# Kernel tuning notes

Measured on AMD Instinct MI355X. Metric: run time of the kernel, lower is better.

Reference implementation:

```python
import jax, jax.numpy as jnp
import numpy as np

N_HEAD, D_K, D_V = 8, 64, 64
TOPK = 16
B, N_R, N_W = 256, 64, 64
D_READ = D_WRITE = D_OUT = 512
TEMP = float(np.power(D_K, 0.5))
EPS = 1e-7  # 10e-8 in original Sparse_attention


def sparse_attention(a, top_k):
    # a: (rows, n); RIMs Sparse_attention: threshold at k-th largest, clamp, renormalize
    if a.shape[-1] <= top_k:
        return a
    delta = jax.lax.top_k(a, top_k)[0][..., -1:] + EPS
    w = jnp.clip(a - delta, 0.0, None)
    return w / (jnp.sum(w, axis=-1, keepdims=True) + EPS)


def setup_inputs() -> dict:
    key = jax.random.key(0)
    ks = jax.random.split(key, 8)
    q = jax.random.normal(ks[0], (B, N_R, D_READ), dtype=jnp.float32)
    k = jax.random.normal(ks[1], (B, N_W, D_WRITE), dtype=jnp.float32)
    v = jax.random.normal(ks[2], (B, N_W, D_WRITE), dtype=jnp.float32)
    # GroupLinearLayer weights: (num_blocks, d_in, n_head*d)
    Wq = 0.02 * jax.random.normal(ks[3], (N_R, D_READ, N_HEAD * D_K), dtype=jnp.float32)
    Wk = 0.02 * jax.random.normal(ks[4], (N_W, D_WRITE, N_HEAD * D_K), dtype=jnp.float32)
    Wv = 0.02 * jax.random.normal(ks[5], (N_W, D_WRITE, N_HEAD * D_V), dtype=jnp.float32)
    fc_w = 0.02 * jax.random.normal(ks[6], (D_OUT, N_HEAD * D_V), dtype=jnp.float32)
    fc_b = jnp.zeros((D_OUT,), dtype=jnp.float32)
    gate_w = 0.02 * jax.random.normal(ks[7], (D_OUT, N_HEAD * D_V), dtype=jnp.float32)
    gate_b = jnp.zeros((D_OUT,), dtype=jnp.float32)
    return {"q": q, "k": k, "v": v, "Wq": Wq, "Wk": Wk, "Wv": Wv,
            "fc_w": fc_w, "fc_b": fc_b, "gate_w": gate_w, "gate_b": gate_b}


def reference(q, k, v, Wq, Wk, Wv, fc_w, fc_b, gate_w, gate_b):
    # grouped per-block projections: out[b,n] = x[b,n] @ W[n]
    qp = jnp.einsum('bnd,nde->bne', q, Wq).reshape(B, N_R, N_HEAD, D_K)
    kp = jnp.einsum('bnd,nde->bne', k, Wk).reshape(B, N_W, N_HEAD, D_K)
    vp = jnp.einsum('bnd,nde->bne', v, Wv).reshape(B, N_W, N_HEAD, D_V)
    # (H*B, len, d) with head-major leading dim, matching permute(2,0,1,3).view(-1,...)
    qh = qp.transpose(2, 0, 1, 3).reshape(N_HEAD * B, N_R, D_K)
    kh = kp.transpose(2, 0, 1, 3).reshape(N_HEAD * B, N_W, D_K)
    vh = vp.transpose(2, 0, 1, 3).reshape(N_HEAD * B, N_W, D_V)
    scores = jnp.einsum('ijk,ilk->ijl', qh, kh) / TEMP          # (HB, Nr, Nw)
    a = jnp.exp(jnp.max(scores, axis=-1, keepdims=True))        # (HB, Nr, 1)
    # flag=True: softmax over the query-block dim (permute/softmax/reshape)
    a = jax.nn.softmax(a[..., 0], axis=-1)                      # (HB, Nr)
    a = sparse_attention(a, TOPK)                               # (HB, Nr)
    attn = a[..., None]                                         # (HB, Nr, 1)
    # einsum 'ijk,ikl->ijl' with attn's k-dim == 1 broadcasts: attn * sum_k v
    out = attn * jnp.sum(vh, axis=1, keepdims=True)             # (HB, Nr, Dv)
    out = out.reshape(N_HEAD, B, N_R, D_V).transpose(1, 2, 0, 3).reshape(B, N_R, N_HEAD * D_V)
    fc_out = out @ fc_w.T + fc_b
    gate = jax.nn.sigmoid(out @ gate_w.T + gate_b)
    output = gate * jnp.tanh(fc_out)                            # residual=True gating
    return output
```

## Files before the change

kernel.cpp:

```cpp
#include <hip/hip_runtime.h>
#include <stdint.h>

#define B_    256
#define NR    64
#define NW    64
#define DIN   512
#define NH    8
#define DK    64
#define E_    512
#define TEMP_INV 0.125f
#define EPSV  1e-7f

typedef unsigned short u16;
typedef unsigned int   u32;
typedef _Float16 f16;
typedef __attribute__((ext_vector_type(2))) float    floatx2;
typedef __attribute__((ext_vector_type(4))) float    floatx4;
typedef __attribute__((ext_vector_type(4))) u32      uintx4;
typedef __attribute__((ext_vector_type(2))) _Float16 halfx2;
typedef __attribute__((ext_vector_type(8))) _Float16 halfx8;

__device__ __forceinline__ halfx2 h2(u32 u) { union { u32 u; halfx2 h; } c; c.u = u; return c.h; }
__device__ __forceinline__ u32 pkh(float a, float b) {
    union { halfx2 h; u32 u; } c; c.h = (halfx2){(f16)a, (f16)b}; return c.u;
}


#define STORE_A(sbuf, pa) do {                                                \
        u32 hh_[8];                                                           \
        _Pragma("unroll")                                                     \
        for (int c = 0; c < 4; c++) {                                         \
            hh_[2*c]   = pkh(pa[c].x, pa[c].y);                               \
            hh_[2*c+1] = pkh(pa[c].z, pa[c].w);                               \
        }                                                                     \
        *(uintx4*)&As[sbuf][(2*ahalf+0)*1024 + arow*8] =                      \
            (uintx4){hh_[0],hh_[1],hh_[2],hh_[3]};                            \
        *(uintx4*)&As[sbuf][(2*ahalf+1)*1024 + arow*8] =                      \
            (uintx4){hh_[4],hh_[5],hh_[6],hh_[7]};                            \
    } while (0)

#define STORE_B(sbuf, pb) do {                                                \
        _Pragma("unroll")                                                     \
        for (int eo = 0; eo < 2; eo++) {                                      \
            uintx4 hv_ = (uintx4){pkh(pb[0][eo], pb[1][eo]),                  \
                                  pkh(pb[2][eo], pb[3][eo]),                  \
                                  pkh(pb[4][eo], pb[5][eo]),                  \
                                  pkh(pb[6][eo], pb[7][eo])};                 \
            *(uintx4*)&Bs[sbuf][kq * 1024 + eo * 512 + p * 8] = hv_;          \
        }                                                                     \
    } while (0)

#define LOAD_A(pa, kn) do {                                                   \
        _Pragma("unroll")                                                     \
        for (int c = 0; c < 4; c++)                                           \
            pa[c] = *(const floatx4*)(aptr + (kn) + c * 4);                   \
    } while (0)

#define LOAD_B(pb, kn) do {                                                   \
        _Pragma("unroll")                                                     \
        for (int j = 0; j < 8; j++)                                           \
            pb[j] = *(const floatx2*)(wptr + (size_t)((kn) + kq*8 + j) * E_); \
    } while (0)

#define COMPUTE(sbuf) do {                                                    \
        halfx8 af_[4], bf_[4];                                                \
        _Pragma("unroll")                                                     \
        for (int mi = 0; mi < 4; mi++)                                        \
            af_[mi] = *(const halfx8*)&As[sbuf][quad*1024 + (wm + mi*16 + l15)*8]; \
        _Pragma("unroll")                                                     \
        for (int ni = 0; ni < 4; ni++) {                                      \
            int e_ = wn + ni*16 + l15;                                        \
            bf_[ni] = *(const halfx8*)&Bs[sbuf][quad*1024 + (e_&1)*512 + (e_>>1)*8]; \
        }                                                                     \
        _Pragma("unroll")                                                     \
        for (int mi = 0; mi < 4; mi++)                                        \
            _Pragma("unroll")                                                 \
            for (int ni = 0; ni < 4; ni++)                                    \
                acc[mi][ni] = __builtin_amdgcn_mfma_f32_16x16x32_f16(         \
                    af_[mi], bf_[ni], acc[mi][ni], 0, 0, 0);                  \
    } while (0)

#define PHASE_BARRIER() do {                                                  \
        asm volatile("s_waitcnt lgkmcnt(0)" ::: "memory");                    \
        __builtin_amdgcn_s_barrier();                                         \
        __builtin_amdgcn_sched_barrier(0);                                    \
    } while (0)

__global__ __launch_bounds__(256, 2)
void proj_kernel(const float* __restrict__ q, const float* __restrict__ kk_,
                 const float* __restrict__ v,
                 const float* __restrict__ Wq, const float* __restrict__ Wk,
                 const float* __restrict__ Wv,
                 f16* __restrict__ qp, f16* __restrict__ kp,
                 f16* __restrict__ vp, float* __restrict__ vsum)
{
    const float* X; const float* W; f16* dst;
    if (blockIdx.z == 0)      { X = q;   W = Wq; dst = qp; }
    else if (blockIdx.z == 1) { X = kk_; W = Wk; dst = kp; }
    else                      { X = v;   W = Wv; dst = vp; }

    const int n  = blockIdx.x * 8 + (blockIdx.y & 7);
    const int t_ = blockIdx.y >> 3;
    const int m0 = (t_ >> 2) * 128;
    const int n0 = (t_ & 3) * 128;

    __shared__ u16 As[2][4096];
    __shared__ u16 Bs[2][4096];

    const int tid  = threadIdx.x;
    const int lane = tid & 63;
    const int wave = tid >> 6;
    const int wm   = (wave >> 1) * 64;
    const int wn   = (wave & 1) * 64;
    const int l15  = lane & 15;
    const int quad = lane >> 4;

    floatx4 acc[4][4];
#pragma unroll
    for (int i = 0; i < 4; i++)
#pragma unroll
        for (int j = 0; j < 4; j++) acc[i][j] = (floatx4){0.f, 0.f, 0.f, 0.f};

    const int arow  = tid >> 1;
    const int ahalf = tid & 1;
    const float* aptr = X + ((size_t)(m0 + arow) * NW + n) * DIN + ahalf * 16;
    const int kq = tid >> 6;
    const int p  = tid & 63;
    const float* wptr = W + (size_t)n * (DIN * E_) + n0 + 2 * p;

    floatx4 pa0[4], pa1[4];
    floatx2 pb0[8], pb1[8];

    LOAD_A(pa0, 0);
    LOAD_A(pa1, 32);
    LOAD_B(pb0, 0);
    LOAD_B(pb1, 32);

#pragma unroll 1
    for (int it2 = 0; it2 < 8; it2++) {
        const int k0 = it2 * 64;
        STORE_A(0, pa0);
        STORE_B(0, pb0);
        if (it2 < 7) { LOAD_A(pa0, k0 + 64); LOAD_B(pb0, k0 + 64); }
        PHASE_BARRIER();
        COMPUTE(0);
        STORE_A(1, pa1);
        STORE_B(1, pb1);
        if (it2 < 7) { LOAD_A(pa1, k0 + 96); LOAD_B(pb1, k0 + 96); }
        PHASE_BARRIER();
        COMPUTE(1);
    }

    if (dst) {
#pragma unroll
        for (int mi = 0; mi < 4; mi++) {
            int rowb = m0 + wm + mi * 16 + quad * 4;
#pragma unroll
            for (int ni = 0; ni < 4; ni++) {
                int col = n0 + wn + ni * 16 + l15;
#pragma unroll
                for (int r = 0; r < 4; r++)
                    dst[((size_t)(rowb + r) * NW + n) * E_ + col] = (f16)acc[mi][ni][r];
            }
        }
    } else {
#pragma unroll
        for (int mi = 0; mi < 4; mi++) {
            int rowb = m0 + wm + mi * 16 + quad * 4;
#pragma unroll
            for (int ni = 0; ni < 4; ni++) {
                int col = n0 + wn + ni * 16 + l15;
#pragma unroll
                for (int r = 0; r < 4; r++)
                    atomicAdd(&vsum[(size_t)(rowb + r) * E_ + col], acc[mi][ni][r]);
            }
        }
    }
}

__global__ __launch_bounds__(256)
void vsum_kernel(const f16* __restrict__ vp, float* __restrict__ vsum)
{
    const int b = blockIdx.x;
    const int t = threadIdx.x;
    const u32* src = (const u32*)vp + (size_t)b * NW * (E_ / 2) + t;
    float s0 = 0.f, s1 = 0.f;
#pragma unroll 4
    for (int nn = 0; nn < NW; nn++) {
        halfx2 hv = h2(src[(size_t)nn * (E_ / 2)]);
        s0 += (float)hv.x;
        s1 += (float)hv.y;
    }
    *(floatx2*)&vsum[(size_t)b * E_ + 2 * t] = (floatx2){s0, s1};
}

__global__ __launch_bounds__(256)
void attn_kernel(const f16* __restrict__ qp, const f16* __restrict__ kp,
                 float* __restrict__ attnT)
{
    const int h = blockIdx.x >> 8;
    const int b = blockIdx.x & 255;
    __shared__ u16 qs[64 * 72];
    __shared__ u16 ks[64 * 72];
    __shared__ float ms[64];

    const int t    = threadIdx.x;
    const int w    = t >> 6;
    const int lane = t & 63;
    const int l15  = lane & 15;
    const int quad = lane >> 4;

    {
        const int r = t >> 2, c = t & 3;
        const f16* qsrc = qp + ((size_t)(b * NR + r)) * E_ + h * DK + c * 16;
        const f16* ksrc = kp + ((size_t)(b * NW + r)) * E_ + h * DK + c * 16;
        *(uintx4*)&qs[r * 72 + c * 16]     = *(const uintx4*)(qsrc);
        *(uintx4*)&qs[r * 72 + c * 16 + 8] = *(const uintx4*)(qsrc + 8);
        *(uintx4*)&ks[r * 72 + c * 16]     = *(const uintx4*)(ksrc);
        *(uintx4*)&ks[r * 72 + c * 16 + 8] = *(const uintx4*)(ksrc + 8);
    }
    __syncthreads();

    floatx4 sc[4];
#pragma unroll
    for (int ni = 0; ni < 4; ni++) sc[ni] = (floatx4){0.f, 0.f, 0.f, 0.f};

    halfx8 af[2];
#pragma unroll
    for (int kk = 0; kk < 2; kk++)
        af[kk] = *(const halfx8*)&qs[(w * 16 + l15) * 72 + kk * 32 + quad * 8];
#pragma unroll
    for (int ni = 0; ni < 4; ni++)
#pragma unroll
        for (int kk = 0; kk < 2; kk++) {
            halfx8 bf = *(const halfx8*)&ks[(ni * 16 + l15) * 72 + kk * 32 + quad * 8];
            sc[ni] = __builtin_amdgcn_mfma_f32_16x16x32_f16(af[kk], bf, sc[ni], 0, 0, 0);
        }

#pragma unroll
    for (int r = 0; r < 4; r++) {
        float rm = fmaxf(fmaxf(sc[0][r], sc[1][r]), fmaxf(sc[2][r], sc[3][r]));
#pragma unroll
        for (int d = 1; d < 16; d <<= 1) rm = fmaxf(rm, __shfl_xor(rm, d));
        if (l15 == 0) ms[w * 16 + quad * 4 + r] = rm;
    }
    __syncthreads();

    if (t < 64) {
        float mm = ms[lane] * TEMP_INV;
        float e = expf(mm);
        float mx = e;
#pragma unroll
        for (int d = 1; d < 64; d <<= 1) mx = fmaxf(mx, __shfl_xor(mx, d));
        float tt = expf(e - mx);
        float S = tt;
#pragma unroll
        for (int d = 1; d < 64; d <<= 1) S += __shfl_xor(S, d);
        float s = tt / S;

        float cur = s, v16 = 0.f;
        for (int itk = 0; itk < 16; itk++) {
            float mv = cur;
#pragma unroll
            for (int d = 1; d < 64; d <<= 1) mv = fmaxf(mv, __shfl_xor(mv, d));
            unsigned long long bal = __ballot(cur == mv);
            int first = __ffsll(bal) - 1;
            if (lane == first) cur = -1e30f;
            v16 = mv;
        }
        float delta = v16 + EPSV;
        float ww = fmaxf(s - delta, 0.f);
        float sw = ww;
#pragma unroll
        for (int d = 1; d < 64; d <<= 1) sw += __shfl_xor(sw, d);
        attnT[((size_t)b * NR + lane) * NH + h] = ww / (sw + EPSV);
    }
}

__global__ __launch_bounds__(256)
void fcv_kernel(const float* __restrict__ vsum, const float* __restrict__ fc_w,
                const float* __restrict__ gate_w, float* __restrict__ fcv,
                float* __restrict__ gatev)
{
    const int ohalf = blockIdx.x >> 3;
    const int bq    = blockIdx.x & 7;
    const int h     = blockIdx.y;
    const float* W  = blockIdx.z ? gate_w : fc_w;
    float* out      = blockIdx.z ? gatev : fcv;
    const int o     = ohalf * 256 + threadIdx.x;

    __shared__ float vs[32 * 64];
#pragma unroll
    for (int i = 0; i < 8; i++) {
        int idx = i * 256 + threadIdx.x;
        int bb = idx >> 6, d = idx & 63;
        vs[idx] = vsum[(size_t)(bq * 32 + bb) * E_ + h * DK + d];
    }
    floatx4 wr[16];
#pragma unroll
    for (int c = 0; c < 16; c++)
        wr[c] = *(const floatx4*)(W + (size_t)o * E_ + h * DK + c * 4);
    __syncthreads();

    for (int bb = 0; bb < 32; bb++) {
        const floatx4* vr = (const floatx4*)&vs[bb * 64];
        float a = 0.f;
#pragma unroll
        for (int c = 0; c < 16; c++) {
            floatx4 vv = vr[c];
            a += vv.x * wr[c].x + vv.y * wr[c].y + vv.z * wr[c].z + vv.w * wr[c].w;
        }
        out[((size_t)(bq * 32 + bb) * NH + h) * E_ + o] = a;
    }
}

__global__ __launch_bounds__(256)
void final_kernel(const float* __restrict__ fcv, const float* __restrict__ gatev,
                  const float* __restrict__ attnT, const float* __restrict__ fc_b,
                  const float* __restrict__ gate_b, float* __restrict__ out)
{
    const int b   = blockIdx.x;
    const int r0  = blockIdx.y * 16;
    const int tid = threadIdx.x;
    __shared__ float ats[16 * NH];

    if (tid < 16 * NH) ats[tid] = attnT[(size_t)b * NR * NH + r0 * NH + tid];

    float fr[2][8], gr[2][8];
#pragma unroll
    for (int half = 0; half < 2; half++) {
        int o = half * 256 + tid;
#pragma unroll
        for (int hh = 0; hh < 8; hh++) {
            fr[half][hh] = fcv[((size_t)b * NH + hh) * E_ + o];
            gr[half][hh] = gatev[((size_t)b * NH + hh) * E_ + o];
        }
    }
    float bfc0 = fc_b[tid],   bfc1 = fc_b[256 + tid];
    float bgt0 = gate_b[tid], bgt1 = gate_b[256 + tid];
    __syncthreads();

    for (int r = 0; r < 16; r++) {
        float a[8];
#pragma unroll
        for (int hh = 0; hh < 8; hh++) a[hh] = ats[r * NH + hh];
#pragma unroll
        for (int half = 0; half < 2; half++) {
            int o = half * 256 + tid;
            float fc = half ? bfc1 : bfc0;
            float gt = half ? bgt1 : bgt0;
#pragma unroll
            for (int hh = 0; hh < 8; hh++) {
                fc = fmaf(a[hh], fr[half][hh], fc);
                gt = fmaf(a[hh], gr[half][hh], gt);
            }
            float g  = 1.f / (1.f + __expf(-gt));
            float e2 = __expf(2.f * fc);
            float th = 1.f - 2.f / (e2 + 1.f);
            out[((size_t)(b * NR + r0 + r)) * E_ + o] = g * th;
        }
    }
}

extern "C" void kernel_launch(void* const* d_in, const int* in_sizes, int n_in,
                              void* d_out, int out_size, void* d_ws, size_t ws_size,
                              hipStream_t stream)
{
    const float* q      = (const float*)d_in[0];
    const float* k      = (const float*)d_in[1];
    const float* v      = (const float*)d_in[2];
    const float* Wq     = (const float*)d_in[3];
    const float* Wk     = (const float*)d_in[4];
    const float* Wv     = (const float*)d_in[5];
    const float* fc_w   = (const float*)d_in[6];
    const float* fc_b   = (const float*)d_in[7];
    const float* gate_w = (const float*)d_in[8];
    const float* gate_b = (const float*)d_in[9];
    float* out = (float*)d_out;

    char* ws = (char*)d_ws;
    f16* qp = (f16*)(ws);
    f16* kp = (f16*)(ws + (16u << 20));

    const bool big = ws_size >= (50u << 20);
    f16* vp; float* vsum; float* attnT; float* fcv; float* gatev;
    if (big) {
        vp    = (f16*)(ws + (32u << 20));
        vsum  = (float*)(ws + (48u << 20));
        attnT = (float*)(ws + (48u << 20) + 524288);
        fcv   = (float*)(ws + (32u << 20));
        gatev = (float*)(ws + (36u << 20));
    } else {
        vp    = nullptr;
        vsum  = (float*)(ws + 33554432);
        attnT = (float*)(ws + 33554432 + 524288);
        fcv   = (float*)(ws + 33554432 + 2 * 524288);
        gatev = (float*)(ws + 33554432 + 2 * 524288 + 4194304);
        hipMemsetAsync(vsum, 0, 524288, stream);
    }

    hipLaunchKernelGGL(proj_kernel, dim3(8, 64, 3), dim3(256), 0, stream,
                       q, k, v, Wq, Wk, Wv, qp, kp, vp, vsum);
    hipLaunchKernelGGL(attn_kernel, dim3(2048), dim3(256), 0, stream, qp, kp, attnT);
    if (big)
        hipLaunchKernelGGL(vsum_kernel, dim3(256), dim3(256), 0, stream, vp, vsum);
    hipLaunchKernelGGL(fcv_kernel, dim3(16, 8, 2), dim3(256), 0, stream,
                       vsum, fc_w, gate_w, fcv, gatev);
    hipLaunchKernelGGL(final_kernel, dim3(256, 4), dim3(256), 0, stream,
                       fcv, gatev, attnT, fc_b, gate_b, out);
}
```

Baseline: 353.1 us.

## Fuse vsum, fc/gate projection and gating epilogue into one tail kernel

```diff
diff --git a/kernel.cpp b/kernel.cpp
--- a/kernel.cpp
+++ b/kernel.cpp
@@ -179,22 +179,6 @@
 }
 
 __global__ __launch_bounds__(256)
-void vsum_kernel(const f16* __restrict__ vp, float* __restrict__ vsum)
-{
-    const int b = blockIdx.x;
-    const int t = threadIdx.x;
-    const u32* src = (const u32*)vp + (size_t)b * NW * (E_ / 2) + t;
-    float s0 = 0.f, s1 = 0.f;
-#pragma unroll 4
-    for (int nn = 0; nn < NW; nn++) {
-        halfx2 hv = h2(src[(size_t)nn * (E_ / 2)]);
-        s0 += (float)hv.x;
-        s1 += (float)hv.y;
-    }
-    *(floatx2*)&vsum[(size_t)b * E_ + 2 * t] = (floatx2){s0, s1};
-}
-
-__global__ __launch_bounds__(256)
 void attn_kernel(const f16* __restrict__ qp, const f16* __restrict__ kp,
                  float* __restrict__ attnT)
 {
@@ -278,87 +262,88 @@
 }
 
 __global__ __launch_bounds__(256)
-void fcv_kernel(const float* __restrict__ vsum, const float* __restrict__ fc_w,
-                const float* __restrict__ gate_w, float* __restrict__ fcv,
-                float* __restrict__ gatev)
+void tail_kernel(const f16* __restrict__ vp, const float* __restrict__ vsum_g,
+                 const float* __restrict__ attnT,
+                 const float* __restrict__ fc_w, const float* __restrict__ gate_w,
+                 const float* __restrict__ fc_b, const float* __restrict__ gate_b,
+                 float* __restrict__ out)
 {
-    const int ohalf = blockIdx.x >> 3;
-    const int bq    = blockIdx.x & 7;
-    const int h     = blockIdx.y;
-    const float* W  = blockIdx.z ? gate_w : fc_w;
-    float* out      = blockIdx.z ? gatev : fcv;
-    const int o     = ohalf * 256 + threadIdx.x;
-
-    __shared__ float vs[32 * 64];
-#pragma unroll
-    for (int i = 0; i < 8; i++) {
-        int idx = i * 256 + threadIdx.x;
-        int bb = idx >> 6, d = idx & 63;
-        vs[idx] = vsum[(size_t)(bq * 32 + bb) * E_ + h * DK + d];
-    }
-    floatx4 wr[16];
-#pragma unroll
-    for (int c = 0; c < 16; c++)
-        wr[c] = *(const floatx4*)(W + (size_t)o * E_ + h * DK + c * 4);
+    const int b    = blockIdx.x;
+    const int t    = threadIdx.x;
+    const int wave = t >> 6;
+    const int lane = t & 63;
+    const int og   = lane >> 2;
+    const int qq   = lane & 3;
+
+    __shared__ float vs[E_];
+    __shared__ float at[NR * NH];
+    __shared__ float fl[NH * E_];
+    __shared__ float gl[NH * E_];
+
+    if (vp) {
+        const u32* src = (const u32*)vp + (size_t)b * NW * (E_ / 2) + t;
+        float s0 = 0.f, s1 = 0.f;
+#pragma unroll 4
+        for (int nn = 0; nn < NW; nn++) {
+            halfx2 hv = h2(src[(size_t)nn * (E_ / 2)]);
+            s0 += (float)hv.x; s1 += (float)hv.y;
+        }
+        vs[2 * t] = s0; vs[2 * t + 1] = s1;
+    } else {
+        *(floatx2*)&vs[2 * t] = *(const floatx2*)&vsum_g[(size_t)b * E_ + 2 * t];
+    }
+    *(floatx2*)&at[2 * t] = *(const floatx2*)&attnT[(size_t)b * NR * NH + 2 * t];
     __syncthreads();
 
-    for (int bb = 0; bb < 32; bb++) {
-        const floatx4* vr = (const floatx4*)&vs[bb * 64];
-        float a = 0.f;
-#pragma unroll
-        for (int c = 0; c < 16; c++) {
-            floatx4 vv = vr[c];
-            a += vv.x * wr[c].x + vv.y * wr[c].y + vv.z * wr[c].z + vv.w * wr[c].w;
-        }
-        out[((size_t)(bq * 32 + bb) * NH + h) * E_ + o] = a;
-    }
-}
-
-__global__ __launch_bounds__(256)
-void final_kernel(const float* __restrict__ fcv, const float* __restrict__ gatev,
-                  const float* __restrict__ attnT, const float* __restrict__ fc_b,
-                  const float* __restrict__ gate_b, float* __restrict__ out)
-{
-    const int b   = blockIdx.x;
-    const int r0  = blockIdx.y * 16;
-    const int tid = threadIdx.x;
-    __shared__ float ats[16 * NH];
-
-    if (tid < 16 * NH) ats[tid] = attnT[(size_t)b * NR * NH + r0 * NH + tid];
-
-    float fr[2][8], gr[2][8];
-#pragma unroll
-    for (int half = 0; half < 2; half++) {
-        int o = half * 256 + tid;
-#pragma unroll
-        for (int hh = 0; hh < 8; hh++) {
-            fr[half][hh] = fcv[((size_t)b * NH + hh) * E_ + o];
-            gr[half][hh] = gatev[((size_t)b * NH + hh) * E_ + o];
-        }
-    }
-    float bfc0 = fc_b[tid],   bfc1 = fc_b[256 + tid];
-    float bgt0 = gate_b[tid], bgt1 = gate_b[256 + tid];
+#pragma unroll 1
+    for (int h = 0; h < NH; h++) {
+        floatx4 vv[4];
+#pragma unroll
+        for (int c = 0; c < 4; c++)
+            vv[c] = *(const floatx4*)&vs[h * 64 + qq * 16 + c * 4];
+#pragma unroll 1
+        for (int ob = 0; ob < 8; ob++) {
+            const int o = wave * 128 + ob * 16 + og;
+            const float* fw = fc_w   + (size_t)o * E_ + h * 64 + qq * 16;
+            const float* gw = gate_w + (size_t)o * E_ + h * 64 + qq * 16;
+            float f = 0.f, g = 0.f;
+#pragma unroll
+            for (int c = 0; c < 4; c++) {
+                floatx4 w0 = *(const floatx4*)(fw + c * 4);
+                floatx4 w1 = *(const floatx4*)(gw + c * 4);
+                f += vv[c].x*w0.x + vv[c].y*w0.y + vv[c].z*w0.z + vv[c].w*w0.w;
+                g += vv[c].x*w1.x + vv[c].y*w1.y + vv[c].z*w1.z + vv[c].w*w1.w;
+            }
+            f += __shfl_xor(f, 1); f += __shfl_xor(f, 2);
+            g += __shfl_xor(g, 1); g += __shfl_xor(g, 2);
+            if (qq == 0) { fl[h * E_ + o] = f; gl[h * E_ + o] = g; }
+        }
+    }
     __syncthreads();
 
-    for (int r = 0; r < 16; r++) {
-        float a[8];
-#pragma unroll
-        for (int hh = 0; hh < 8; hh++) a[hh] = ats[r * NH + hh];
-#pragma unroll
-        for (int half = 0; half < 2; half++) {
-            int o = half * 256 + tid;
-            float fc = half ? bfc1 : bfc0;
-            float gt = half ? bgt1 : bgt0;
-#pragma unroll
-            for (int hh = 0; hh < 8; hh++) {
-                fc = fmaf(a[hh], fr[half][hh], fc);
-                gt = fmaf(a[hh], gr[half][hh], gt);
-            }
-            float g  = 1.f / (1.f + __expf(-gt));
-            float e2 = __expf(2.f * fc);
-            float th = 1.f - 2.f / (e2 + 1.f);
-            out[((size_t)(b * NR + r0 + r)) * E_ + o] = g * th;
-        }
+    float fr0[NH], fr1[NH], gr0[NH], gr1[NH];
+#pragma unroll
+    for (int h = 0; h < NH; h++) {
+        floatx2 a0 = *(const floatx2*)&fl[h * E_ + 2 * t];
+        floatx2 a1 = *(const floatx2*)&gl[h * E_ + 2 * t];
+        fr0[h] = a0.x; fr1[h] = a0.y; gr0[h] = a1.x; gr1[h] = a1.y;
+    }
+    const float bf0 = fc_b[2 * t],   bf1 = fc_b[2 * t + 1];
+    const float bg0 = gate_b[2 * t], bg1 = gate_b[2 * t + 1];
+#pragma unroll 2
+    for (int r = 0; r < NR; r++) {
+        float fc0 = bf0, fc1 = bf1, gt0 = bg0, gt1 = bg1;
+#pragma unroll
+        for (int h = 0; h < NH; h++) {
+            float a = at[r * NH + h];
+            fc0 = fmaf(a, fr0[h], fc0); fc1 = fmaf(a, fr1[h], fc1);
+            gt0 = fmaf(a, gr0[h], gt0); gt1 = fmaf(a, gr1[h], gt1);
+        }
+        float g0 = 1.f / (1.f + __expf(-gt0));
+        float g1 = 1.f / (1.f + __expf(-gt1));
+        float e0 = __expf(2.f * fc0), e1 = __expf(2.f * fc1);
+        float th0 = 1.f - 2.f / (e0 + 1.f), th1 = 1.f - 2.f / (e1 + 1.f);
+        *(floatx2*)&out[((size_t)(b * NR + r)) * E_ + 2 * t] = (floatx2){g0 * th0, g1 * th1};
     }
 }
 
@@ -383,29 +368,21 @@
     f16* kp = (f16*)(ws + (16u << 20));
 
     const bool big = ws_size >= (50u << 20);
-    f16* vp; float* vsum; float* attnT; float* fcv; float* gatev;
+    f16* vp; float* vsum; float* attnT;
     if (big) {
         vp    = (f16*)(ws + (32u << 20));
         vsum  = (float*)(ws + (48u << 20));
         attnT = (float*)(ws + (48u << 20) + 524288);
-        fcv   = (float*)(ws + (32u << 20));
-        gatev = (float*)(ws + (36u << 20));
     } else {
         vp    = nullptr;
         vsum  = (float*)(ws + 33554432);
         attnT = (float*)(ws + 33554432 + 524288);
-        fcv   = (float*)(ws + 33554432 + 2 * 524288);
-        gatev = (float*)(ws + 33554432 + 2 * 524288 + 4194304);
         hipMemsetAsync(vsum, 0, 524288, stream);
     }
 
     hipLaunchKernelGGL(proj_kernel, dim3(8, 64, 3), dim3(256), 0, stream,
                        q, k, v, Wq, Wk, Wv, qp, kp, vp, vsum);
     hipLaunchKernelGGL(attn_kernel, dim3(2048), dim3(256), 0, stream, qp, kp, attnT);
-    if (big)
-        hipLaunchKernelGGL(vsum_kernel, dim3(256), dim3(256), 0, stream, vp, vsum);
-    hipLaunchKernelGGL(fcv_kernel, dim3(16, 8, 2), dim3(256), 0, stream,
-                       vsum, fc_w, gate_w, fcv, gatev);
-    hipLaunchKernelGGL(final_kernel, dim3(256, 4), dim3(256), 0, stream,
-                       fcv, gatev, attnT, fc_b, gate_b, out);
-}
+    hipLaunchKernelGGL(tail_kernel, dim3(256), dim3(256), 0, stream,
+                       vp, vsum, attnT, fc_w, gate_w, fc_b, gate_b, out);
+}
```

Measured after the change: 381.4 us. 1.08x slower.
